# Optimization experiments

Hardware: AMD Instinct MI355X
Metric: run time of the kernel (lower is better)

Reference implementation:

```python
import jax, jax.numpy as jnp
import numpy as np

H = 8        # n_head
F = 512      # feature_dim
K = 64       # key_feature_dim
TEMP = 30.0
EPS = 1e-12  # torch F.normalize eps


def _l2norm(x):
    # normalize over last axis, matching torch.nn.functional.normalize(p=2, dim=-1)
    n = jnp.sqrt(jnp.sum(x * x, axis=-1, keepdims=True))
    return x / jnp.maximum(n, EPS)


def setup_inputs() -> dict:
    k0 = jax.random.key(0)
    kq, kk, kv, kw = jax.random.split(k0, 4)
    Lq, Lk, B = 1024, 1024, 16
    query = jax.random.normal(kq, (Lq, B, F), dtype=jnp.float32)
    key = jax.random.normal(kk, (Lk, B, F), dtype=jnp.float32)
    value = jax.random.normal(kv, (Lk, B, F), dtype=jnp.float32)
    # per-head WK: weight ~ N(0, sqrt(2/out_features)), bias = 0
    Wk = jax.random.normal(kw, (H, K, F), dtype=jnp.float32) * np.float32(np.sqrt(2.0 / K))
    bk = jnp.zeros((H, K), dtype=jnp.float32)
    return {"query": query, "key": key, "value": value, "Wk": Wk, "bk": bk}


def reference(query, key, value, Wk, bk):
    # query/key/value: [L, B, F]; Wk: [H, K, F]; bk: [H, K]
    wq = _l2norm(jnp.einsum('qbf,hkf->qbhk', query, Wk) + bk)  # [Lq,B,H,K]
    wk = _l2norm(jnp.einsum('sbf,hkf->sbhk', key, Wk) + bk)    # [Lk,B,H,K]
    scores = jnp.einsum('qbhk,sbhk->bhqs', wq, wk) * TEMP      # [B,H,Lq,Lk]
    attn = jax.nn.softmax(scores, axis=-1)
    # NOTE: original forward uses raw `value` (WV is defined but never applied)
    out = jnp.einsum('bhqs,sbf->qbhf', attn, value)            # [Lq,B,H,F]
    Lq, B = out.shape[0], out.shape[1]
    return out.reshape(Lq, B, H * F)  # concat over heads on last dim
```

## Files before the change

kernel.cpp:

```cpp
#include <hip/hip_runtime.h>
#include <cstdint>
#include <cstddef>


typedef _Float16 half8 __attribute__((ext_vector_type(8)));
typedef _Float16 half4v __attribute__((ext_vector_type(4)));
typedef float floatx4 __attribute__((ext_vector_type(4)));

#define MFMA16(a, b, c) __builtin_amdgcn_mfma_f32_16x16x32_f16((a), (b), (c), 0, 0, 0)

static constexpr int LQn = 1024;
static constexpr int LKn = 1024;
static constexpr int Bn  = 16;
static constexpr int Fn  = 512;
static constexpr int Kn  = 64;
static constexpr int Hn  = 8;

__global__ __launch_bounds__(256) void vt_kernel(const float* __restrict__ V,
                                                 _Float16* __restrict__ Vt) {
    __shared__ __align__(16) _Float16 tile[64][72];
    int idx = blockIdx.x;
    int b  = idx >> 7;
    int r  = idx & 127;
    int s0 = (r >> 3) << 6;
    int f0 = (r & 7) << 6;
    int t  = threadIdx.x;
    int cg = t & 15;
    int rg = t >> 4;

#pragma unroll
    for (int p = 0; p < 4; ++p) {
        int s = rg + p * 16;
        const float* src = V + (((size_t)(s0 + s) * Bn + b) * Fn + f0 + cg * 4);
        floatx4 v = *(const floatx4*)src;
        half4v hv;
        hv[0] = (_Float16)v[0]; hv[1] = (_Float16)v[1];
        hv[2] = (_Float16)v[2]; hv[3] = (_Float16)v[3];
        *(half4v*)&tile[s][cg * 4] = hv;
    }
    __syncthreads();
#pragma unroll
    for (int p = 0; p < 4; ++p) {
        int f  = rg + p * 16;
        int sb = cg * 4;
        half4v hv;
        hv[0] = tile[sb + 0][f]; hv[1] = tile[sb + 1][f];
        hv[2] = tile[sb + 2][f]; hv[3] = tile[sb + 3][f];
        *(half4v*)(Vt + ((size_t)(b * Fn + f0 + f) * LKn + s0 + sb)) = hv;
    }
}

__global__ __launch_bounds__(256) void proj_kernel(const float* __restrict__ Q,
                                                   const float* __restrict__ Kin,
                                                   const float* __restrict__ W,
                                                   _Float16* __restrict__ wq,
                                                   _Float16* __restrict__ wk) {
    __shared__ __align__(16) _Float16 At[128 * 64];
    __shared__ __align__(16) _Float16 Bt[128 * 64];

    int idx   = blockIdx.x;
    int nt    = idx & 3;
    int mt    = idx >> 2;
    int tileM = mt << 7;
    int tileN = nt << 7;
    bool isQ  = (tileM < 16384);
    const float* Asrc = isQ ? (Q + (size_t)tileM * Fn)
                            : (Kin + (size_t)(tileM - 16384) * Fn);

    int t    = threadIdx.x;
    int w    = t >> 6;
    int lane = t & 63;
    int quad = lane >> 4;
    int l16  = lane & 15;
    int mrow = (w & 1) * 64;
    int ncol = (w >> 1) * 64;

    floatx4 acc[4][4] = {};

    for (int k0 = 0; k0 < Fn; k0 += 64) {
#pragma unroll
        for (int p = 0; p < 4; ++p) {
            int slot = p * 256 + t;
            int row  = slot >> 3;
            int kc   = slot & 7;
            const float* g = Asrc + (size_t)row * Fn + k0 + kc * 8;
            floatx4 v0 = *(const floatx4*)g;
            floatx4 v1 = *(const floatx4*)(g + 4);
            half8 hv;
            hv[0] = (_Float16)v0[0]; hv[1] = (_Float16)v0[1];
            hv[2] = (_Float16)v0[2]; hv[3] = (_Float16)v0[3];
            hv[4] = (_Float16)v1[0]; hv[5] = (_Float16)v1[1];
            hv[6] = (_Float16)v1[2]; hv[7] = (_Float16)v1[3];
            *(half8*)&At[row * 64 + ((kc ^ (row & 7)) << 3)] = hv;
        }
#pragma unroll
        for (int p = 0; p < 4; ++p) {
            int slot = p * 256 + t;
            int row  = slot >> 3;
            int kc   = slot & 7;
            const float* g = W + (size_t)(tileN + row) * Fn + k0 + kc * 8;
            floatx4 v0 = *(const floatx4*)g;
            floatx4 v1 = *(const floatx4*)(g + 4);
            half8 hv;
            hv[0] = (_Float16)v0[0]; hv[1] = (_Float16)v0[1];
            hv[2] = (_Float16)v0[2]; hv[3] = (_Float16)v0[3];
            hv[4] = (_Float16)v1[0]; hv[5] = (_Float16)v1[1];
            hv[6] = (_Float16)v1[2]; hv[7] = (_Float16)v1[3];
            *(half8*)&Bt[row * 64 + ((kc ^ (row & 7)) << 3)] = hv;
        }
        __syncthreads();

#pragma unroll
        for (int c = 0; c < 2; ++c) {
            half8 af[4], bf[4];
#pragma unroll
            for (int mi = 0; mi < 4; ++mi) {
                int row = mrow + mi * 16 + l16;
                af[mi] = *(half8*)&At[row * 64 + (((c * 4 + quad) ^ (row & 7)) << 3)];
            }
#pragma unroll
            for (int ni = 0; ni < 4; ++ni) {
                int row = ncol + ni * 16 + l16;
                bf[ni] = *(half8*)&Bt[row * 64 + (((c * 4 + quad) ^ (row & 7)) << 3)];
            }
#pragma unroll
            for (int mi = 0; mi < 4; ++mi)
#pragma unroll
                for (int ni = 0; ni < 4; ++ni)
                    acc[mi][ni] = MFMA16(af[mi], bf[ni], acc[mi][ni]);
        }
        __syncthreads();
    }

    _Float16* dst0  = isQ ? wq : wk;
    int   tbase     = isQ ? tileM : (tileM - 16384);
    float tscale    = isQ ? 30.0f : 1.0f;

#pragma unroll
    for (int mi = 0; mi < 4; ++mi) {
        float rs[4];
#pragma unroll
        for (int r = 0; r < 4; ++r) {
            float s = 0.f;
#pragma unroll
            for (int ni = 0; ni < 4; ++ni) {
                float v = acc[mi][ni][r];
                s += v * v;
            }
            s += __shfl_xor(s, 1);
            s += __shfl_xor(s, 2);
            s += __shfl_xor(s, 4);
            s += __shfl_xor(s, 8);
            rs[r] = tscale / fmaxf(sqrtf(s), 1e-12f);
        }
#pragma unroll
        for (int ni = 0; ni < 4; ++ni) {
            int col = tileN + ncol + ni * 16 + l16;
            int hh  = col >> 6;
            int kk  = col & 63;
#pragma unroll
            for (int r = 0; r < 4; ++r) {
                int trow = tbase + mrow + mi * 16 + quad * 4 + r;
                int l    = trow >> 4;
                int bb   = trow & 15;
                dst0[((size_t)(bb * Hn + hh) * LQn + l) * Kn + kk] =
                    (_Float16)(acc[mi][ni][r] * rs[r]);
            }
        }
    }
}

__global__ __launch_bounds__(512) void attn_kernel(const _Float16* __restrict__ wq,
                                                   const _Float16* __restrict__ wk,
                                                   const _Float16* __restrict__ Vt,
                                                   float* __restrict__ out) {
    __shared__ __align__(16) float    Sbuf[64 * 68];
    __shared__ __align__(16) _Float16 Pbuf[64 * 72];
    __shared__ __align__(16) float    mbuf[64];
    __shared__ __align__(16) float    lbuf[64];
    __shared__ __align__(16) float    abuf[64];

    int idx = blockIdx.x;
    int bh  = idx & 127;
    int qt  = idx >> 7;
    int b   = bh >> 3;
    int h   = bh & 7;
    int q0  = qt << 6;

    int t    = threadIdx.x;
    int w    = t >> 6;
    int lane = t & 63;
    int quad = lane >> 4;
    int l16  = lane & 15;

    const _Float16* wqb = wq + (size_t)bh * LQn * Kn;
    const _Float16* wkb = wk + (size_t)bh * LKn * Kn;
    const _Float16* vb  = Vt + (size_t)b * Fn * LKn;

    int qi  = w >> 1;
    int sih = (w & 1) * 2;
    int fsl = w * 64;

    half8 qf[2];
#pragma unroll
    for (int c = 0; c < 2; ++c)
        qf[c] = *(const half8*)(wqb + (size_t)(q0 + qi * 16 + l16) * Kn + c * 32 + quad * 8);

    floatx4 O[4][4] = {};
    if (t < 64) { mbuf[t] = -1e30f; lbuf[t] = 0.f; }
    __syncthreads();

    for (int it = 0; it < 16; ++it) {
        int s0 = it << 6;

        half8 vf[4][2];
#pragma unroll
        for (int fi = 0; fi < 4; ++fi)
#pragma unroll
            for (int c = 0; c < 2; ++c)
                vf[fi][c] = *(const half8*)(vb + (size_t)(fsl + fi * 16 + l16) * LKn +
                                            s0 + c * 32 + quad * 8);

#pragma unroll
        for (int sj = 0; sj < 2; ++sj) {
            floatx4 sacc = {};
#pragma unroll
            for (int c = 0; c < 2; ++c) {
                half8 kf = *(const half8*)(wkb + (size_t)(s0 + (sih + sj) * 16 + l16) * Kn +
                                           c * 32 + quad * 8);
                sacc = MFMA16(qf[c], kf, sacc);
            }
            int col = (sih + sj) * 16 + l16;
#pragma unroll
            for (int r = 0; r < 4; ++r)
                Sbuf[(qi * 16 + quad * 4 + r) * 68 + col] = sacc[r];
        }
        __syncthreads();

        {
            int rr = t >> 3, g = t & 7;
            float* srow = &Sbuf[rr * 68 + g * 8];
            floatx4 x0 = *(floatx4*)srow;
            floatx4 x1 = *(floatx4*)(srow + 4);
            float tmax = fmaxf(fmaxf(fmaxf(x0[0], x0[1]), fmaxf(x0[2], x0[3])),
                               fmaxf(fmaxf(x1[0], x1[1]), fmaxf(x1[2], x1[3])));
            tmax = fmaxf(tmax, __shfl_xor(tmax, 1));
            tmax = fmaxf(tmax, __shfl_xor(tmax, 2));
            tmax = fmaxf(tmax, __shfl_xor(tmax, 4));
            float mo = mbuf[rr];
            float mn = fmaxf(mo, tmax);
            float p0 = __expf(x0[0] - mn), p1 = __expf(x0[1] - mn);
            float p2 = __expf(x0[2] - mn), p3 = __expf(x0[3] - mn);
            float p4 = __expf(x1[0] - mn), p5 = __expf(x1[1] - mn);
            float p6 = __expf(x1[2] - mn), p7 = __expf(x1[3] - mn);
            float ps = ((p0 + p1) + (p2 + p3)) + ((p4 + p5) + (p6 + p7));
            ps += __shfl_xor(ps, 1);
            ps += __shfl_xor(ps, 2);
            ps += __shfl_xor(ps, 4);
            float al = __expf(mo - mn);
            if (g == 0) {
                mbuf[rr] = mn;
                lbuf[rr] = lbuf[rr] * al + ps;
                abuf[rr] = al;
            }
            half8 ph;
            ph[0] = (_Float16)p0; ph[1] = (_Float16)p1; ph[2] = (_Float16)p2; ph[3] = (_Float16)p3;
            ph[4] = (_Float16)p4; ph[5] = (_Float16)p5; ph[6] = (_Float16)p6; ph[7] = (_Float16)p7;
            *(half8*)&Pbuf[rr * 72 + g * 8] = ph;
        }
        __syncthreads();

#pragma unroll
        for (int q2 = 0; q2 < 4; ++q2) {
            floatx4 al = *(floatx4*)&abuf[q2 * 16 + quad * 4];
#pragma unroll
            for (int fi = 0; fi < 4; ++fi)
#pragma unroll
                for (int r = 0; r < 4; ++r)
                    O[q2][fi][r] *= al[r];
        }
#pragma unroll
        for (int c = 0; c < 2; ++c) {
            half8 pf[4];
#pragma unroll
            for (int q2 = 0; q2 < 4; ++q2)
                pf[q2] = *(half8*)&Pbuf[(q2 * 16 + l16) * 72 + c * 32 + quad * 8];
#pragma unroll
            for (int q2 = 0; q2 < 4; ++q2)
#pragma unroll
                for (int fi = 0; fi < 4; ++fi)
                    O[q2][fi] = MFMA16(pf[q2], vf[fi][c], O[q2][fi]);
        }
        __syncthreads();
    }

#pragma unroll
    for (int q2 = 0; q2 < 4; ++q2) {
        floatx4 lv = *(floatx4*)&lbuf[q2 * 16 + quad * 4];
#pragma unroll
        for (int fi = 0; fi < 4; ++fi) {
#pragma unroll
            for (int r = 0; r < 4; ++r) {
                int row = q0 + q2 * 16 + quad * 4 + r;
                int col = h * Fn + fsl + fi * 16 + l16;
                out[((size_t)row * Bn + b) * (Hn * Fn) + col] = O[q2][fi][r] / lv[r];
            }
        }
    }
}

extern "C" void kernel_launch(void* const* d_in, const int* in_sizes, int n_in,
                              void* d_out, int out_size, void* d_ws, size_t ws_size,
                              hipStream_t stream) {
    const float* query = (const float*)d_in[0];
    const float* key   = (const float*)d_in[1];
    const float* value = (const float*)d_in[2];
    const float* Wk    = (const float*)d_in[3];
    float* out = (float*)d_out;

    char* ws = (char*)d_ws;
    _Float16* wq = (_Float16*)ws;
    _Float16* wk = (_Float16*)(ws + (size_t)(1 << 24));
    _Float16* Vt = (_Float16*)(ws + (size_t)(2 << 24));

    hipLaunchKernelGGL(vt_kernel, dim3(2048), dim3(256), 0, stream, value, Vt);
    hipLaunchKernelGGL(proj_kernel, dim3(1024), dim3(256), 0, stream, query, key, Wk, wq, wk);
    hipLaunchKernelGGL(attn_kernel, dim3(2048), dim3(512), 0, stream, wq, wk, Vt, out);
}
```

Measured before the change: 780.8 us.

## Precompute exact row max, drop online softmax rescale, double-buffer K via LDS

The attention kernel now computes the full row max of the scores in a first pass, so the main loop needs no running-max rescaling of the output accumulator and no separate shared score buffer with its extra barrier. K tiles are prefetched into double-buffered shared memory with direct global-to-LDS loads, and blocks are remapped so each XCD handles contiguous batches for better L2 reuse. The projection kernel is retiled so each block computes all 8 heads for 64 rows with 512 threads, which means W is converted once per k-step and the per-row normalization spans the block. The cost is a duplicated QK^T pass for the max and higher register and LDS pressure.

Result: slower. 929.8 us (+19.1%).

```diff
diff --git a/kernel.cpp b/kernel.cpp
--- a/kernel.cpp
+++ b/kernel.cpp
@@ -9,8 +9,12 @@
 
 #define MFMA16(a, b, c) __builtin_amdgcn_mfma_f32_16x16x32_f16((a), (b), (c), 0, 0, 0)
 
+#define GLOAD_LDS16(g, l)                                                     \
+    __builtin_amdgcn_global_load_lds(                                         \
+        (const __attribute__((address_space(1))) void*)(g),                   \
+        (__attribute__((address_space(3))) void*)(l), 16, 0, 0)
+
 static constexpr int LQn = 1024;
-static constexpr int LKn = 1024;
 static constexpr int Bn  = 16;
 static constexpr int Fn  = 512;
 static constexpr int Kn  = 64;
@@ -46,43 +50,38 @@
         half4v hv;
         hv[0] = tile[sb + 0][f]; hv[1] = tile[sb + 1][f];
         hv[2] = tile[sb + 2][f]; hv[3] = tile[sb + 3][f];
-        *(half4v*)(Vt + ((size_t)(b * Fn + f0 + f) * LKn + s0 + sb)) = hv;
+        *(half4v*)(Vt + ((size_t)(b * Fn + f0 + f) * LQn + s0 + sb)) = hv;
     }
 }
 
-__global__ __launch_bounds__(256) void proj_kernel(const float* __restrict__ Q,
-                                                   const float* __restrict__ Kin,
-                                                   const float* __restrict__ W,
-                                                   _Float16* __restrict__ wq,
-                                                   _Float16* __restrict__ wk) {
-    __shared__ __align__(16) _Float16 At[128 * 64];
-    __shared__ __align__(16) _Float16 Bt[128 * 64];
+__global__ __launch_bounds__(512, 4) void proj_kernel(const float* __restrict__ Q,
+                                                      const float* __restrict__ Kin,
+                                                      const float* __restrict__ W,
+                                                      _Float16* __restrict__ wq,
+                                                      _Float16* __restrict__ wk) {
+    __shared__ __align__(16) _Float16 At[64 * 64];
+    __shared__ __align__(16) _Float16 Bt[512 * 64];
 
     int idx   = blockIdx.x;
-    int nt    = idx & 3;
-    int mt    = idx >> 2;
-    int tileM = mt << 7;
-    int tileN = nt << 7;
-    bool isQ  = (tileM < 16384);
-    const float* Asrc = isQ ? (Q + (size_t)tileM * Fn)
-                            : (Kin + (size_t)(tileM - 16384) * Fn);
+    bool isQ  = idx < 256;
+    int tbase = (idx & 255) << 6;
+    const float* Asrc = isQ ? (Q + (size_t)tbase * Fn)
+                            : (Kin + (size_t)tbase * Fn);
 
     int t    = threadIdx.x;
     int w    = t >> 6;
     int lane = t & 63;
     int quad = lane >> 4;
     int l16  = lane & 15;
-    int mrow = (w & 1) * 64;
-    int ncol = (w >> 1) * 64;
-
-    floatx4 acc[4][4] = {};
+    int mrow = (w & 1) * 32;
+    int ncol = (w >> 1) * 128;
+
+    floatx4 acc[2][8] = {};
 
     for (int k0 = 0; k0 < Fn; k0 += 64) {
-#pragma unroll
-        for (int p = 0; p < 4; ++p) {
-            int slot = p * 256 + t;
-            int row  = slot >> 3;
-            int kc   = slot & 7;
+        {
+            int row = t >> 3;
+            int kc  = t & 7;
             const float* g = Asrc + (size_t)row * Fn + k0 + kc * 8;
             floatx4 v0 = *(const floatx4*)g;
             floatx4 v1 = *(const floatx4*)(g + 4);
@@ -94,11 +93,11 @@
             *(half8*)&At[row * 64 + ((kc ^ (row & 7)) << 3)] = hv;
         }
 #pragma unroll
-        for (int p = 0; p < 4; ++p) {
-            int slot = p * 256 + t;
+        for (int p = 0; p < 8; ++p) {
+            int slot = p * 512 + t;
             int row  = slot >> 3;
             int kc   = slot & 7;
-            const float* g = W + (size_t)(tileN + row) * Fn + k0 + kc * 8;
+            const float* g = W + (size_t)row * Fn + k0 + kc * 8;
             floatx4 v0 = *(const floatx4*)g;
             floatx4 v1 = *(const floatx4*)(g + 4);
             half8 hv;
@@ -112,50 +111,52 @@
 
 #pragma unroll
         for (int c = 0; c < 2; ++c) {
-            half8 af[4], bf[4];
-#pragma unroll
-            for (int mi = 0; mi < 4; ++mi) {
+            half8 af[2], bf[8];
+#pragma unroll
+            for (int mi = 0; mi < 2; ++mi) {
                 int row = mrow + mi * 16 + l16;
                 af[mi] = *(half8*)&At[row * 64 + (((c * 4 + quad) ^ (row & 7)) << 3)];
             }
 #pragma unroll
-            for (int ni = 0; ni < 4; ++ni) {
+            for (int ni = 0; ni < 8; ++ni) {
                 int row = ncol + ni * 16 + l16;
                 bf[ni] = *(half8*)&Bt[row * 64 + (((c * 4 + quad) ^ (row & 7)) << 3)];
             }
 #pragma unroll
-            for (int mi = 0; mi < 4; ++mi)
-#pragma unroll
-                for (int ni = 0; ni < 4; ++ni)
+            for (int mi = 0; mi < 2; ++mi)
+#pragma unroll
+                for (int ni = 0; ni < 8; ++ni)
                     acc[mi][ni] = MFMA16(af[mi], bf[ni], acc[mi][ni]);
         }
         __syncthreads();
     }
 
-    _Float16* dst0  = isQ ? wq : wk;
-    int   tbase     = isQ ? tileM : (tileM - 16384);
-    float tscale    = isQ ? 30.0f : 1.0f;
-
-#pragma unroll
-    for (int mi = 0; mi < 4; ++mi) {
-        float rs[4];
+    _Float16* dst = isQ ? wq : wk;
+    float tsc     = isQ ? 30.0f : 1.0f;
+
+#pragma unroll
+    for (int mi = 0; mi < 2; ++mi) {
+        float rs[2][4];
 #pragma unroll
         for (int r = 0; r < 4; ++r) {
-            float s = 0.f;
+            float s0 = 0.f, s1 = 0.f;
 #pragma unroll
             for (int ni = 0; ni < 4; ++ni) {
-                float v = acc[mi][ni][r];
-                s += v * v;
-            }
-            s += __shfl_xor(s, 1);
-            s += __shfl_xor(s, 2);
-            s += __shfl_xor(s, 4);
-            s += __shfl_xor(s, 8);
-            rs[r] = tscale / fmaxf(sqrtf(s), 1e-12f);
-        }
-#pragma unroll
-        for (int ni = 0; ni < 4; ++ni) {
-            int col = tileN + ncol + ni * 16 + l16;
+                float v0 = acc[mi][ni][r];
+                float v1 = acc[mi][ni + 4][r];
+                s0 += v0 * v0;
+                s1 += v1 * v1;
+            }
+            s0 += __shfl_xor(s0, 1); s1 += __shfl_xor(s1, 1);
+            s0 += __shfl_xor(s0, 2); s1 += __shfl_xor(s1, 2);
+            s0 += __shfl_xor(s0, 4); s1 += __shfl_xor(s1, 4);
+            s0 += __shfl_xor(s0, 8); s1 += __shfl_xor(s1, 8);
+            rs[0][r] = tsc / fmaxf(sqrtf(s0), 1e-12f);
+            rs[1][r] = tsc / fmaxf(sqrtf(s1), 1e-12f);
+        }
+#pragma unroll
+        for (int ni = 0; ni < 8; ++ni) {
+            int col = ncol + ni * 16 + l16;
             int hh  = col >> 6;
             int kk  = col & 63;
 #pragma unroll
@@ -163,147 +164,177 @@
                 int trow = tbase + mrow + mi * 16 + quad * 4 + r;
                 int l    = trow >> 4;
                 int bb   = trow & 15;
-                dst0[((size_t)(bb * Hn + hh) * LQn + l) * Kn + kk] =
-                    (_Float16)(acc[mi][ni][r] * rs[r]);
+                dst[((size_t)(bb * Hn + hh) * LQn + l) * Kn + kk] =
+                    (_Float16)(acc[mi][ni][r] * rs[ni >> 2][r]);
             }
         }
     }
 }
 
-__global__ __launch_bounds__(512) void attn_kernel(const _Float16* __restrict__ wq,
-                                                   const _Float16* __restrict__ wk,
-                                                   const _Float16* __restrict__ Vt,
-                                                   float* __restrict__ out) {
-    __shared__ __align__(16) float    Sbuf[64 * 68];
-    __shared__ __align__(16) _Float16 Pbuf[64 * 72];
-    __shared__ __align__(16) float    mbuf[64];
-    __shared__ __align__(16) float    lbuf[64];
-    __shared__ __align__(16) float    abuf[64];
-
-    int idx = blockIdx.x;
-    int bh  = idx & 127;
-    int qt  = idx >> 7;
-    int b   = bh >> 3;
-    int h   = bh & 7;
-    int q0  = qt << 6;
-
-    int t    = threadIdx.x;
-    int w    = t >> 6;
-    int lane = t & 63;
-    int quad = lane >> 4;
-    int l16  = lane & 15;
+__global__ __launch_bounds__(512, 4) void attn_kernel(const _Float16* __restrict__ wq,
+                                                      const _Float16* __restrict__ wk,
+                                                      const _Float16* __restrict__ Vt,
+                                                      float* __restrict__ out) {
+    __shared__ __align__(16) _Float16 ktile[2][64 * 64];
+    __shared__ __align__(16) _Float16 Pbuf[2][64 * 72];
+    __shared__ __align__(16) float    mpart[8 * 64];
+    __shared__ __align__(16) float    mfin[64];
+    __shared__ __align__(16) float    lpart[2 * 64];
+
+    const floatx4 z4 = {};
+
+    int n    = blockIdx.x;
+    int xcd  = n & 7;
+    int rank = n >> 3;
+    int b    = xcd * 2 + (rank >> 7);
+    int h    = (rank >> 4) & 7;
+    int qt   = rank & 15;
+    int q0   = qt << 6;
+    int bh   = b * Hn + h;
+
+    int t     = threadIdx.x;
+    int w     = t >> 6;
+    int lane  = t & 63;
+    int quad  = lane >> 4;
+    int l16   = lane & 15;
+    int qsub  = w >> 1;
+    int shalf = w & 1;
+    int fsl   = w << 6;
 
     const _Float16* wqb = wq + (size_t)bh * LQn * Kn;
-    const _Float16* wkb = wk + (size_t)bh * LKn * Kn;
-    const _Float16* vb  = Vt + (size_t)b * Fn * LKn;
-
-    int qi  = w >> 1;
-    int sih = (w & 1) * 2;
-    int fsl = w * 64;
-
-    half8 qf[2];
-#pragma unroll
-    for (int c = 0; c < 2; ++c)
-        qf[c] = *(const half8*)(wqb + (size_t)(q0 + qi * 16 + l16) * Kn + c * 32 + quad * 8);
+    const _Float16* wkb = wk + (size_t)bh * LQn * Kn;
+    const _Float16* vb  = Vt + (size_t)b * Fn * LQn;
+
+    half8 qa[4][2];
+#pragma unroll
+    for (int g = 0; g < 4; ++g)
+#pragma unroll
+        for (int c = 0; c < 2; ++c)
+            qa[g][c] = *(const half8*)(wqb + (size_t)(q0 + g * 16 + l16) * Kn +
+                                       c * 32 + quad * 8);
+
+    floatx4 vmax[4];
+#pragma unroll
+    for (int g = 0; g < 4; ++g) {
+        vmax[g][0] = -1e30f; vmax[g][1] = -1e30f;
+        vmax[g][2] = -1e30f; vmax[g][3] = -1e30f;
+    }
+
+    for (int u = 0; u < 8; ++u) {
+        int srow = (w << 7) + (u << 4) + l16;
+        half8 ka0 = *(const half8*)(wkb + (size_t)srow * Kn + quad * 8);
+        half8 ka1 = *(const half8*)(wkb + (size_t)srow * Kn + 32 + quad * 8);
+#pragma unroll
+        for (int g = 0; g < 4; ++g) {
+            floatx4 f = MFMA16(ka0, qa[g][0], z4);
+            f = MFMA16(ka1, qa[g][1], f);
+#pragma unroll
+            for (int r = 0; r < 4; ++r) vmax[g][r] = fmaxf(vmax[g][r], f[r]);
+        }
+    }
+#pragma unroll
+    for (int g = 0; g < 4; ++g) {
+        float mg = fmaxf(fmaxf(vmax[g][0], vmax[g][1]), fmaxf(vmax[g][2], vmax[g][3]));
+        mg = fmaxf(mg, __shfl_xor(mg, 16));
+        mg = fmaxf(mg, __shfl_xor(mg, 32));
+        if (lane < 16) mpart[w * 64 + g * 16 + lane] = mg;
+    }
+    __syncthreads();
+    if (t < 64) {
+        float mm = mpart[t];
+#pragma unroll
+        for (int w2 = 1; w2 < 8; ++w2) mm = fmaxf(mm, mpart[w2 * 64 + t]);
+        mfin[t] = mm;
+    }
+    GLOAD_LDS16(wkb + (size_t)(w * 8) * Kn + lane * 8, &ktile[0][w * 8 * 64]);
+    __syncthreads();
+
+    float nm = -mfin[qsub * 16 + l16];
+    half8 qf0 = qa[qsub][0];
+    half8 qf1 = qa[qsub][1];
 
     floatx4 O[4][4] = {};
-    if (t < 64) { mbuf[t] = -1e30f; lbuf[t] = 0.f; }
+    floatx4 lsum = {};
+
+#pragma unroll 2
+    for (int it = 0; it < 16; ++it) {
+        int tb = it & 1;
+        int s0 = it << 6;
+
+        half8 vf0[4];
+#pragma unroll
+        for (int fi = 0; fi < 4; ++fi)
+            vf0[fi] = *(const half8*)(vb + (size_t)(fsl + fi * 16 + l16) * LQn +
+                                      s0 + quad * 8);
+
+        int s0n = (it == 15) ? s0 : (s0 + 64);
+        GLOAD_LDS16(wkb + (size_t)(s0n + w * 8) * Kn + lane * 8,
+                    &ktile[tb ^ 1][w * 8 * 64]);
+
+#pragma unroll
+        for (int ss = 0; ss < 2; ++ss) {
+            int sL = (shalf * 2 + ss) * 16 + l16;
+            half8 kf0 = *(const half8*)&ktile[tb][sL * 64 + quad * 8];
+            half8 kf1 = *(const half8*)&ktile[tb][sL * 64 + 32 + quad * 8];
+            floatx4 sacc = MFMA16(kf0, qf0, z4);
+            sacc = MFMA16(kf1, qf1, sacc);
+            float p0 = __expf(sacc[0] + nm);
+            float p1 = __expf(sacc[1] + nm);
+            float p2 = __expf(sacc[2] + nm);
+            float p3 = __expf(sacc[3] + nm);
+            lsum[0] += p0; lsum[1] += p1; lsum[2] += p2; lsum[3] += p3;
+            half4v pk;
+            pk[0] = (_Float16)p0; pk[1] = (_Float16)p1;
+            pk[2] = (_Float16)p2; pk[3] = (_Float16)p3;
+            *(half4v*)&Pbuf[tb][(qsub * 16 + l16) * 72 +
+                                (shalf * 2 + ss) * 16 + quad * 4] = pk;
+        }
+        __syncthreads();
+
+#pragma unroll
+        for (int c = 0; c < 2; ++c) {
+            half8 vfc[4];
+            if (c == 0) {
+#pragma unroll
+                for (int fi = 0; fi < 4; ++fi) vfc[fi] = vf0[fi];
+            } else {
+#pragma unroll
+                for (int fi = 0; fi < 4; ++fi)
+                    vfc[fi] = *(const half8*)(vb + (size_t)(fsl + fi * 16 + l16) * LQn +
+                                              s0 + 32 + quad * 8);
+            }
+            half8 pf[4];
+#pragma unroll
+            for (int g = 0; g < 4; ++g)
+                pf[g] = *(half8*)&Pbuf[tb][(g * 16 + l16) * 72 + c * 32 + quad * 8];
+#pragma unroll
+            for (int g = 0; g < 4; ++g)
+#pragma unroll
+                for (int fi = 0; fi < 4; ++fi)
+                    O[g][fi] = MFMA16(pf[g], vfc[fi], O[g][fi]);
+        }
+    }
+
+    float ls = lsum[0] + lsum[1] + lsum[2] + lsum[3];
+    ls += __shfl_xor(ls, 16);
+    ls += __shfl_xor(ls, 32);
+    if (lane < 16) lpart[shalf * 64 + qsub * 16 + lane] = ls;
     __syncthreads();
 
-    for (int it = 0; it < 16; ++it) {
-        int s0 = it << 6;
-
-        half8 vf[4][2];
-#pragma unroll
-        for (int fi = 0; fi < 4; ++fi)
-#pragma unroll
-            for (int c = 0; c < 2; ++c)
-                vf[fi][c] = *(const half8*)(vb + (size_t)(fsl + fi * 16 + l16) * LKn +
-                                            s0 + c * 32 + quad * 8);
-
-#pragma unroll
-        for (int sj = 0; sj < 2; ++sj) {
-            floatx4 sacc = {};
-#pragma unroll
-            for (int c = 0; c < 2; ++c) {
-                half8 kf = *(const half8*)(wkb + (size_t)(s0 + (sih + sj) * 16 + l16) * Kn +
-                                           c * 32 + quad * 8);
-                sacc = MFMA16(qf[c], kf, sacc);
-            }
-            int col = (sih + sj) * 16 + l16;
-#pragma unroll
-            for (int r = 0; r < 4; ++r)
-                Sbuf[(qi * 16 + quad * 4 + r) * 68 + col] = sacc[r];
-        }
-        __syncthreads();
-
-        {
-            int rr = t >> 3, g = t & 7;
-            float* srow = &Sbuf[rr * 68 + g * 8];
-            floatx4 x0 = *(floatx4*)srow;
-            floatx4 x1 = *(floatx4*)(srow + 4);
-            float tmax = fmaxf(fmaxf(fmaxf(x0[0], x0[1]), fmaxf(x0[2], x0[3])),
-                               fmaxf(fmaxf(x1[0], x1[1]), fmaxf(x1[2], x1[3])));
-            tmax = fmaxf(tmax, __shfl_xor(tmax, 1));
-            tmax = fmaxf(tmax, __shfl_xor(tmax, 2));
-            tmax = fmaxf(tmax, __shfl_xor(tmax, 4));
-            float mo = mbuf[rr];
-            float mn = fmaxf(mo, tmax);
-            float p0 = __expf(x0[0] - mn), p1 = __expf(x0[1] - mn);
-            float p2 = __expf(x0[2] - mn), p3 = __expf(x0[3] - mn);
-            float p4 = __expf(x1[0] - mn), p5 = __expf(x1[1] - mn);
-            float p6 = __expf(x1[2] - mn), p7 = __expf(x1[3] - mn);
-            float ps = ((p0 + p1) + (p2 + p3)) + ((p4 + p5) + (p6 + p7));
-            ps += __shfl_xor(ps, 1);
-            ps += __shfl_xor(ps, 2);
-            ps += __shfl_xor(ps, 4);
-            float al = __expf(mo - mn);
-            if (g == 0) {
-                mbuf[rr] = mn;
-                lbuf[rr] = lbuf[rr] * al + ps;
-                abuf[rr] = al;
-            }
-            half8 ph;
-            ph[0] = (_Float16)p0; ph[1] = (_Float16)p1; ph[2] = (_Float16)p2; ph[3] = (_Float16)p3;
-            ph[4] = (_Float16)p4; ph[5] = (_Float16)p5; ph[6] = (_Float16)p6; ph[7] = (_Float16)p7;
-            *(half8*)&Pbuf[rr * 72 + g * 8] = ph;
-        }
-        __syncthreads();
-
-#pragma unroll
-        for (int q2 = 0; q2 < 4; ++q2) {
-            floatx4 al = *(floatx4*)&abuf[q2 * 16 + quad * 4];
-#pragma unroll
-            for (int fi = 0; fi < 4; ++fi)
-#pragma unroll
-                for (int r = 0; r < 4; ++r)
-                    O[q2][fi][r] *= al[r];
-        }
-#pragma unroll
-        for (int c = 0; c < 2; ++c) {
-            half8 pf[4];
-#pragma unroll
-            for (int q2 = 0; q2 < 4; ++q2)
-                pf[q2] = *(half8*)&Pbuf[(q2 * 16 + l16) * 72 + c * 32 + quad * 8];
-#pragma unroll
-            for (int q2 = 0; q2 < 4; ++q2)
-#pragma unroll
-                for (int fi = 0; fi < 4; ++fi)
-                    O[q2][fi] = MFMA16(pf[q2], vf[fi][c], O[q2][fi]);
-        }
-        __syncthreads();
-    }
-
-#pragma unroll
-    for (int q2 = 0; q2 < 4; ++q2) {
-        floatx4 lv = *(floatx4*)&lbuf[q2 * 16 + quad * 4];
+#pragma unroll
+    for (int g = 0; g < 4; ++g) {
+        floatx4 l0 = *(floatx4*)&lpart[g * 16 + quad * 4];
+        floatx4 l1 = *(floatx4*)&lpart[64 + g * 16 + quad * 4];
+        floatx4 linv;
+#pragma unroll
+        for (int r = 0; r < 4; ++r) linv[r] = __builtin_amdgcn_rcpf(l0[r] + l1[r]);
 #pragma unroll
         for (int fi = 0; fi < 4; ++fi) {
 #pragma unroll
             for (int r = 0; r < 4; ++r) {
-                int row = q0 + q2 * 16 + quad * 4 + r;
+                int row = q0 + g * 16 + quad * 4 + r;
                 int col = h * Fn + fsl + fi * 16 + l16;
-                out[((size_t)row * Bn + b) * (Hn * Fn) + col] = O[q2][fi][r] / lv[r];
+                out[((size_t)row * Bn + b) * (Hn * Fn) + col] = O[g][fi][r] * linv[r];
             }
         }
     }
@@ -324,6 +355,6 @@
     _Float16* Vt = (_Float16*)(ws + (size_t)(2 << 24));
 
     hipLaunchKernelGGL(vt_kernel, dim3(2048), dim3(256), 0, stream, value, Vt);
-    hipLaunchKernelGGL(proj_kernel, dim3(1024), dim3(256), 0, stream, query, key, Wk, wq, wk);
+    hipLaunchKernelGGL(proj_kernel, dim3(512), dim3(512), 0, stream, query, key, Wk, wq, wk);
     hipLaunchKernelGGL(attn_kernel, dim3(2048), dim3(512), 0, stream, wq, wk, Vt, out);
 }
```
